# Kernel optimization log

Measured on AMD Instinct MI355X. Metric: run time of the kernel, lower is better.

Reference implementation:

```python
import jax, jax.numpy as jnp
import numpy as np

MAX_DISP = 4                 # max_displacement
OUT_DIM = 2 * MAX_DISP + 1   # 9 -> 81 displacement channels


def setup_inputs() -> dict:
    key = jax.random.key(0)
    k1, k2 = jax.random.split(key)
    B, C, H, W = 8, 64, 192, 192
    x1 = jax.random.normal(k1, (B, C, H, W), dtype=jnp.float32)
    x2 = jax.random.normal(k2, (B, C, H, W), dtype=jnp.float32)
    return {"x1": x1, "x2": x2}


def reference(x1, x2):
    # x1, x2: [B, C, H, W]; stride1 = stride2 = 1 (default-equivalent config)
    B, C, H, W = x1.shape
    # pad x2 by max_displacement on each spatial side
    x2p = jnp.pad(x2, ((0, 0), (0, 0), (MAX_DISP, MAX_DISP), (MAX_DISP, MAX_DISP)))
    # for each displacement (i, j): channel-mean of x1 * shifted window of x2
    cv = [
        jnp.mean(x1 * jax.lax.dynamic_slice(x2p, (0, 0, i, j), (B, C, H, W)), axis=1)
        for i in range(OUT_DIM)
        for j in range(OUT_DIM)
    ]
    # torch.cat of keepdim means == stack along channel: [B, OUT_DIM**2, H, W]
    return jnp.stack(cv, axis=1)
```

## Files before the change

kernel.cpp:

```cpp
#include <hip/hip_runtime.h>


constexpr int MAXD = 4;
constexpr int OD   = 9;
constexpr int ND   = 81;
constexpr int TB_W = 32;
constexpr int TB_H = 16;
constexpr int TWp  = 8;
constexpr int CK   = 4;
constexpr int NW   = 3;
constexpr int NT   = NW * 64;
constexpr int XROWS = TB_H + NW - 1;
constexpr int XSTR  = 44;

constexpr int Bc = 8, Cc = 64, Hc = 192, Wc = 192;
constexpr int HW = Hc * Wc;
constexpr int NCH   = Cc / CK;
constexpr int CSTEP = CK * HW;
constexpr int F4_PER_CH = XROWS * XSTR / 4;
constexpr int SLAB_F4_REAL = CK * F4_PER_CH;
constexpr int SLOTS = 5;
constexpr int SLAB_F4 = SLOTS * NT;
constexpr int SLAB_F  = SLAB_F4 * 4;

constexpr int GX = Wc / TB_W;
constexpr int GY = Hc / TB_H;
constexpr int NBLK = GX * GY * Bc * 3;

__device__ __align__(16) float g_zero4[4];

__device__ inline void gload_lds16(const float* g, float* l) {
    __builtin_amdgcn_global_load_lds(
        (const __attribute__((address_space(1))) void*)g,
        (__attribute__((address_space(3))) void*)l, 16, 0, 0);
}

__global__ __launch_bounds__(NT, 2) void corr_kernel(
    const float* __restrict__ x1, const float* __restrict__ x2,
    float* __restrict__ out)
{
    __shared__ __align__(16) float s2[2][SLAB_F];

    const int tid  = threadIdx.x;
    const int lane = tid & 63;
    const int wid  = tid >> 6;
    const int px8  = (lane & 3) * 8;
    const int gh   = lane >> 2;

    const int n    = blockIdx.x;
    const int b    = n & 7;
    const int t    = n >> 3;
    const int g3   = t % 3;
    const int tile = t / 3;
    const int ty   = tile / GX;
    const int tx   = tile - ty * GX;
    const int w0   = tx * TB_W;
    const int h0   = ty * TB_H;
    const int di   = 3 * g3 + wid;

    const float* x1b = x1 + (long)b * Cc * HW;
    const float* x2b = x2 + (long)b * Cc * HW;

    int  q[SLOTS];
    int  d4[SLOTS];
    bool ok[SLOTS];
#pragma unroll
    for (int i = 0; i < SLOTS; ++i) {
        int s = wid * (SLOTS * 64) + i * 64 + lane;
        d4[i] = s * 4;
        int sr = (s < SLAB_F4_REAL) ? s : 0;
        int c  = sr / F4_PER_CH;
        int rm = sr - c * F4_PER_CH;
        int r  = rm / (XSTR / 4);
        int x4 = rm - r * (XSTR / 4);
        int rg = h0 + 3 * g3 - MAXD + r;
        int gc = w0 - MAXD + x4 * 4;
        ok[i] = (s < SLAB_F4_REAL) && (x4 < 10) &&
                ((unsigned)rg < (unsigned)Hc) && ((unsigned)gc < (unsigned)(Wc - 3));
        q[i]  = c * HW + rg * Wc + gc;
    }

    float acc[OD][TWp];
#pragma unroll
    for (int dj = 0; dj < OD; ++dj)
#pragma unroll
        for (int p = 0; p < TWp; ++p) acc[dj][p] = 0.f;

    int poff = (h0 + gh) * Wc + (w0 + px8);
    const int ldr = gh + wid;

    auto stage = [&](int k, float* buf) {
        const int cb = k * CSTEP;
        const float* z = g_zero4;
#pragma unroll
        for (int i = 0; i < SLOTS; ++i)
            gload_lds16(ok[i] ? x2b + cb + q[i] : z, buf + d4[i]);
    };

    stage(0, s2[0]);
    __syncthreads();

#pragma unroll 1
    for (int k = 0; k < NCH; ++k) {
        float* bufA = s2[k & 1];
        float* bufB = s2[(k & 1) ^ 1];

        if (k + 1 < NCH) stage(k + 1, bufB);

#pragma unroll
        for (int c = 0; c < CK; ++c) {
            float4 a0 = *(const float4*)(x1b + poff);
            float4 a1 = *(const float4*)(x1b + poff + 4);
            poff += HW;
            const float* wr = bufA + c * (XROWS * XSTR) + ldr * XSTR + px8;
            float4 b0 = *(const float4*)(wr);
            float4 b1 = *(const float4*)(wr + 4);
            float4 b2 = *(const float4*)(wr + 8);
            float4 b3 = *(const float4*)(wr + 12);
            float win[16] = {b0.x, b0.y, b0.z, b0.w,  b1.x, b1.y, b1.z, b1.w,
                             b2.x, b2.y, b2.z, b2.w,  b3.x, b3.y, b3.z, b3.w};
            float av[8]  = {a0.x, a0.y, a0.z, a0.w,  a1.x, a1.y, a1.z, a1.w};
#pragma unroll
            for (int dj = 0; dj < OD; ++dj)
#pragma unroll
                for (int p = 0; p < TWp; ++p)
                    acc[dj][p] = fmaf(av[p], win[p + dj], acc[dj][p]);
        }

        __syncthreads();
    }

    const float scale = 1.0f / 64.0f;
    float* ob = out + (((long)b * ND + di * OD) * Hc + (h0 + gh)) * Wc + (w0 + px8);
#pragma unroll
    for (int dj = 0; dj < OD; ++dj) {
        float4 v0, v1;
        v0.x = acc[dj][0] * scale;  v0.y = acc[dj][1] * scale;
        v0.z = acc[dj][2] * scale;  v0.w = acc[dj][3] * scale;
        v1.x = acc[dj][4] * scale;  v1.y = acc[dj][5] * scale;
        v1.z = acc[dj][6] * scale;  v1.w = acc[dj][7] * scale;
        *(float4*)(ob + (long)dj * HW)     = v0;
        *(float4*)(ob + (long)dj * HW + 4) = v1;
    }
}

extern "C" void kernel_launch(void* const* d_in, const int* in_sizes, int n_in,
                              void* d_out, int out_size, void* d_ws, size_t ws_size,
                              hipStream_t stream) {
    const float* x1 = (const float*)d_in[0];
    const float* x2 = (const float*)d_in[1];
    float* out = (float*)d_out;
    corr_kernel<<<dim3(NBLK), NT, 0, stream>>>(x1, x2, out);
}
```

Measured before the change: 300.9 us.

## Drop LDS staging and read x2 windows directly from global memory per wave

Removes the double-buffered LDS slab filled by global_load_lds, and with it the block-wide barriers. Each wave now owns one displacement row for one tile and loads its x2 window straight from global memory with clamped addresses. Out-of-bounds padding is handled by zeroing those outputs at store time instead of loading zeros. The trade-off is more global and L2 traffic, since overlapping x2 windows are no longer shared between waves, in exchange for no synchronisation and simpler per-wave scheduling at 4 waves per block.

Measured after the change: 340.6 us. +13.2%, slower.

```diff
diff --git a/kernel.cpp b/kernel.cpp
--- a/kernel.cpp
+++ b/kernel.cpp
@@ -7,78 +7,51 @@
 constexpr int TB_W = 32;
 constexpr int TB_H = 16;
 constexpr int TWp  = 8;
-constexpr int CK   = 4;
-constexpr int NW   = 3;
-constexpr int NT   = NW * 64;
-constexpr int XROWS = TB_H + NW - 1;
-constexpr int XSTR  = 44;
+constexpr int NT   = 256;
 
 constexpr int Bc = 8, Cc = 64, Hc = 192, Wc = 192;
 constexpr int HW = Hc * Wc;
-constexpr int NCH   = Cc / CK;
-constexpr int CSTEP = CK * HW;
-constexpr int F4_PER_CH = XROWS * XSTR / 4;
-constexpr int SLAB_F4_REAL = CK * F4_PER_CH;
-constexpr int SLOTS = 5;
-constexpr int SLAB_F4 = SLOTS * NT;
-constexpr int SLAB_F  = SLAB_F4 * 4;
-
 constexpr int GX = Wc / TB_W;
 constexpr int GY = Hc / TB_H;
-constexpr int NBLK = GX * GY * Bc * 3;
-
-__device__ __align__(16) float g_zero4[4];
-
-__device__ inline void gload_lds16(const float* g, float* l) {
-    __builtin_amdgcn_global_load_lds(
-        (const __attribute__((address_space(1))) void*)g,
-        (__attribute__((address_space(3))) void*)l, 16, 0, 0);
-}
+constexpr int NTILE = GX * GY;
+constexpr int UPI   = NTILE * OD;
+constexpr int NBLK  = Bc * UPI / 4;
 
 __global__ __launch_bounds__(NT, 2) void corr_kernel(
     const float* __restrict__ x1, const float* __restrict__ x2,
     float* __restrict__ out)
 {
-    __shared__ __align__(16) float s2[2][SLAB_F];
-
     const int tid  = threadIdx.x;
     const int lane = tid & 63;
     const int wid  = tid >> 6;
     const int px8  = (lane & 3) * 8;
     const int gh   = lane >> 2;
 
-    const int n    = blockIdx.x;
-    const int b    = n & 7;
-    const int t    = n >> 3;
-    const int g3   = t % 3;
-    const int tile = t / 3;
+    const int B    = blockIdx.x;
+    const int b    = B & 7;
+    const int up   = (B >> 3) * 4 + wid;
+    const int di   = up % OD;
+    const int tile = up / OD;
     const int ty   = tile / GX;
     const int tx   = tile - ty * GX;
     const int w0   = tx * TB_W;
     const int h0   = ty * TB_H;
-    const int di   = 3 * g3 + wid;
 
     const float* x1b = x1 + (long)b * Cc * HW;
     const float* x2b = x2 + (long)b * Cc * HW;
 
-    int  q[SLOTS];
-    int  d4[SLOTS];
-    bool ok[SLOTS];
-#pragma unroll
-    for (int i = 0; i < SLOTS; ++i) {
-        int s = wid * (SLOTS * 64) + i * 64 + lane;
-        d4[i] = s * 4;
-        int sr = (s < SLAB_F4_REAL) ? s : 0;
-        int c  = sr / F4_PER_CH;
-        int rm = sr - c * F4_PER_CH;
-        int r  = rm / (XSTR / 4);
-        int x4 = rm - r * (XSTR / 4);
-        int rg = h0 + 3 * g3 - MAXD + r;
-        int gc = w0 - MAXD + x4 * 4;
-        ok[i] = (s < SLAB_F4_REAL) && (x4 < 10) &&
-                ((unsigned)rg < (unsigned)Hc) && ((unsigned)gc < (unsigned)(Wc - 3));
-        q[i]  = c * HW + rg * Wc + gc;
-    }
+    const int r1 = h0 + gh;
+    const int cb = w0 + px8;
+    const int rg = r1 + di - MAXD;
+    const bool rowok = (unsigned)rg < (unsigned)Hc;
+    const int rgc = min(max(rg, 0), Hc - 1);
+    const int cc0 = (cb >= 4) ? (cb - 4) : 0;
+    const int cc3 = (cb <= Wc - 12) ? (cb + 8) : (Wc - 4);
+
+    const int o1 = r1  * Wc + cb;
+    const int e0 = rgc * Wc + cc0;
+    const int e1 = rgc * Wc + cb;
+    const int e3 = rgc * Wc + cc3;
 
     float acc[OD][TWp];
 #pragma unroll
@@ -86,59 +59,38 @@
 #pragma unroll
         for (int p = 0; p < TWp; ++p) acc[dj][p] = 0.f;
 
-    int poff = (h0 + gh) * Wc + (w0 + px8);
-    const int ldr = gh + wid;
-
-    auto stage = [&](int k, float* buf) {
-        const int cb = k * CSTEP;
-        const float* z = g_zero4;
+#pragma unroll 4
+    for (int c = 0; c < Cc; ++c) {
+        const float* p1 = x1b + c * HW;
+        const float* p2 = x2b + c * HW;
+        float4 a0 = *(const float4*)(p1 + o1);
+        float4 a1 = *(const float4*)(p1 + o1 + 4);
+        float4 q0 = *(const float4*)(p2 + e0);
+        float4 q1 = *(const float4*)(p2 + e1);
+        float4 q2 = *(const float4*)(p2 + e1 + 4);
+        float4 q3 = *(const float4*)(p2 + e3);
+        float wn[16] = {q0.x,q0.y,q0.z,q0.w,  q1.x,q1.y,q1.z,q1.w,
+                        q2.x,q2.y,q2.z,q2.w,  q3.x,q3.y,q3.z,q3.w};
+        float av[8]  = {a0.x,a0.y,a0.z,a0.w,  a1.x,a1.y,a1.z,a1.w};
 #pragma unroll
-        for (int i = 0; i < SLOTS; ++i)
-            gload_lds16(ok[i] ? x2b + cb + q[i] : z, buf + d4[i]);
-    };
-
-    stage(0, s2[0]);
-    __syncthreads();
-
-#pragma unroll 1
-    for (int k = 0; k < NCH; ++k) {
-        float* bufA = s2[k & 1];
-        float* bufB = s2[(k & 1) ^ 1];
-
-        if (k + 1 < NCH) stage(k + 1, bufB);
-
+        for (int dj = 0; dj < OD; ++dj)
 #pragma unroll
-        for (int c = 0; c < CK; ++c) {
-            float4 a0 = *(const float4*)(x1b + poff);
-            float4 a1 = *(const float4*)(x1b + poff + 4);
-            poff += HW;
-            const float* wr = bufA + c * (XROWS * XSTR) + ldr * XSTR + px8;
-            float4 b0 = *(const float4*)(wr);
-            float4 b1 = *(const float4*)(wr + 4);
-            float4 b2 = *(const float4*)(wr + 8);
-            float4 b3 = *(const float4*)(wr + 12);
-            float win[16] = {b0.x, b0.y, b0.z, b0.w,  b1.x, b1.y, b1.z, b1.w,
-                             b2.x, b2.y, b2.z, b2.w,  b3.x, b3.y, b3.z, b3.w};
-            float av[8]  = {a0.x, a0.y, a0.z, a0.w,  a1.x, a1.y, a1.z, a1.w};
-#pragma unroll
-            for (int dj = 0; dj < OD; ++dj)
-#pragma unroll
-                for (int p = 0; p < TWp; ++p)
-                    acc[dj][p] = fmaf(av[p], win[p + dj], acc[dj][p]);
-        }
-
-        __syncthreads();
+            for (int p = 0; p < TWp; ++p)
+                acc[dj][p] = fmaf(av[p], wn[p + dj], acc[dj][p]);
     }
 
-    const float scale = 1.0f / 64.0f;
-    float* ob = out + (((long)b * ND + di * OD) * Hc + (h0 + gh)) * Wc + (w0 + px8);
+    const float sc = 1.0f / 64.0f;
+    float* ob = out + (((long)b * ND + di * OD) * Hc + r1) * Wc + cb;
 #pragma unroll
     for (int dj = 0; dj < OD; ++dj) {
-        float4 v0, v1;
-        v0.x = acc[dj][0] * scale;  v0.y = acc[dj][1] * scale;
-        v0.z = acc[dj][2] * scale;  v0.w = acc[dj][3] * scale;
-        v1.x = acc[dj][4] * scale;  v1.y = acc[dj][5] * scale;
-        v1.z = acc[dj][6] * scale;  v1.w = acc[dj][7] * scale;
+        float v[TWp];
+#pragma unroll
+        for (int p = 0; p < TWp; ++p) {
+            const bool ok = rowok && ((unsigned)(cb + p + dj - MAXD) < (unsigned)Wc);
+            v[p] = ok ? acc[dj][p] * sc : 0.f;
+        }
+        float4 v0 = {v[0], v[1], v[2], v[3]};
+        float4 v1 = {v[4], v[5], v[6], v[7]};
         *(float4*)(ob + (long)dj * HW)     = v0;
         *(float4*)(ob + (long)dj * HW + 4) = v1;
     }
```
